# Optimization experiments

Measured on AMD Instinct MI355X. Metric: run time of the kernel, lower is better.

The kernel has to match this reference:

```python
import jax, jax.numpy as jnp
import numpy as np
from jax import lax

# Problem dims (match init_kwargs / input_specs)
B, C, H, W = 4, 256, 64, 64
G, KH, KW, PAD = 8, 3, 3, 1
KK = KH * KW
CG = C // G  # channels per group


def setup_inputs() -> dict:
    key = jax.random.key(0)
    k0, k1, k2, k3, k4 = jax.random.split(key, 5)
    x = jax.random.normal(k0, (B, C, H, W), jnp.float32)
    # offset predictor conv: Conv2d(C, 2*KK*G, 3, padding=1); small init keeps offsets moderate
    offset_w = jax.random.normal(k1, (2 * KK * G, C, 3, 3), jnp.float32) * 0.01
    offset_b = jax.random.normal(k2, (2 * KK * G,), jnp.float32) * 0.01
    # deformable grouped conv weight: [C_out=C, C_in//G, KH, KW]
    fan_in = CG * KK
    deform_w = jax.random.normal(k3, (C, CG, KH, KW), jnp.float32) / np.sqrt(fan_in).astype(np.float32)
    deform_b = jax.random.normal(k4, (C,), jnp.float32) * 0.01
    return {"x": x, "offset_w": offset_w, "offset_b": offset_b,
            "deform_w": deform_w, "deform_b": deform_b}


def _deform_group_conv(x, offset_w, offset_b, deform_w, deform_b):
    # 1) predict offsets with a plain 3x3 conv
    offset = lax.conv_general_dilated(
        x, offset_w, window_strides=(1, 1), padding=((PAD, PAD), (PAD, PAD)),
        dimension_numbers=("NCHW", "OIHW", "NCHW")) + offset_b[None, :, None, None]

    # torchvision layout: [B, G, KK, (dy,dx), H, W]
    off = offset.reshape(B, G, KK, 2, H, W)
    off_y, off_x = off[:, :, :, 0], off[:, :, :, 1]  # [B,G,KK,H,W]

    dt = x.dtype
    hh = jnp.arange(H, dtype=dt)[None, None, None, :, None]
    ww = jnp.arange(W, dtype=dt)[None, None, None, None, :]
    ki = (jnp.arange(KK) // KW).astype(dt)[None, None, :, None, None]
    kj = (jnp.arange(KK) % KW).astype(dt)[None, None, :, None, None]
    # sampling coords for each (kernel tap, output location): [B,G,KK,H,W]
    py = hh - PAD + ki + off_y
    px = ww - PAD + kj + off_x

    y0f, x0f = jnp.floor(py), jnp.floor(px)
    wy1, wx1 = py - y0f, px - x0f
    wy0, wx0 = 1.0 - wy1, 1.0 - wx1
    iy0, ix0 = y0f.astype(jnp.int32), x0f.astype(jnp.int32)

    x_g = x.reshape(B, G, CG, H * W)
    # gather over flattened spatial dim, vmapped over (B, G)
    gather = jax.vmap(jax.vmap(lambda xf, idx: jnp.take(xf, idx, axis=1)))

    def corner(iy, ix, wgt):
        valid = (iy >= 0) & (iy < H) & (ix >= 0) & (ix < W)  # zero padding outside
        idx = (jnp.clip(iy, 0, H - 1) * W + jnp.clip(ix, 0, W - 1)).reshape(B, G, -1)
        w = (wgt * valid.astype(wgt.dtype)).reshape(B, G, 1, -1)
        return gather(x_g, idx) * w  # [B,G,CG,KK*H*W]

    sampled = (corner(iy0,     ix0,     wy0 * wx0)
             + corner(iy0,     ix0 + 1, wy0 * wx1)
             + corner(iy0 + 1, ix0,     wy1 * wx0)
             + corner(iy0 + 1, ix0 + 1, wy1 * wx1))
    sampled = sampled.reshape(B, G, CG, KK, H, W)

    # grouped conv as an einsum over (in-channels-per-group, kernel taps)
    w_g = deform_w.reshape(G, C // G, CG, KK)  # [G, out/g, in/g, KK]
    out = jnp.einsum("gock,bgckhw->bgohw", w_g, sampled).reshape(B, C, H, W)
    return out + deform_b[None, :, None, None]


def reference(x, offset_w, offset_b, deform_w, deform_b):
    return _deform_group_conv(x, offset_w, offset_b, deform_w, deform_b)
```

## Files before the change

kernel.cpp:

```cpp
#include <hip/hip_runtime.h>
#include <hip/hip_bf16.h>
#include <cstddef>
#include <cstdint>

#define CH_HW 4096

typedef __bf16  bf16x8  __attribute__((ext_vector_type(8)));
typedef float   f32x4   __attribute__((ext_vector_type(4)));
typedef unsigned int u32x4 __attribute__((ext_vector_type(4)));

#define WF_ELEMS 331776
#define WF_BYTES (WF_ELEMS * 2)
#define OFFW_BYTES (4u * 144u * CH_HW * 2u)
#define DWB_ELEMS (8 * 9 * 2 * 512)
#define DWB_BYTES (DWB_ELEMS * 2)
#define XT_BYTES ((size_t)4 * 8 * CH_HW * 32 * 2)

__device__ __forceinline__ u32x4 pack_bf16x8(const float av[8]) {
    u32x4 ad;
#pragma unroll
    for (int jj = 0; jj < 4; ++jj) {
        const unsigned int lo = __builtin_bit_cast(unsigned short, __float2bfloat16(av[2 * jj]));
        const unsigned int hi = __builtin_bit_cast(unsigned short, __float2bfloat16(av[2 * jj + 1]));
        ad[jj] = lo | (hi << 16);
    }
    return ad;
}
__device__ __forceinline__ float bf16lo(unsigned int u) {
    return __builtin_bit_cast(float, u << 16);
}
__device__ __forceinline__ float bf16hi(unsigned int u) {
    return __builtin_bit_cast(float, u & 0xFFFF0000u);
}

__global__ __launch_bounds__(256) void prep(const float* __restrict__ ow,
                                            const float* __restrict__ dw,
                                            const float* __restrict__ x,
                                            __hip_bfloat16* __restrict__ wf,
                                            __hip_bfloat16* __restrict__ dwb,
                                            __hip_bfloat16* __restrict__ xt)
{
    const int job = blockIdx.y;
    if (job == 0) {
        const int t = blockIdx.x * 256 + threadIdx.x;
        if (t >= WF_ELEMS) return;
        const int j    = t & 7;
        const int lane = (t >> 3) & 63;
        const int tmp  = t >> 9;
        const int nt   = tmp % 9;
        const int ks   = tmp / 9;
        const int tap  = ks >> 3, icb = ks & 7;
        const int oc   = nt * 16 + (lane & 15);
        const int ic   = icb * 32 + (lane >> 4) * 8 + j;
        wf[t] = __float2bfloat16(ow[(size_t)oc * 2304 + ic * 9 + tap]);
    } else if (job == 1) {
        const int t = blockIdx.x * 256 + threadIdx.x;
        if (t >= DWB_ELEMS) return;
        const int j    = t & 7;
        const int lane = (t >> 3) & 63;
        const int nt   = (t >> 9) & 1;
        const int gk   = t >> 10;
        const int k    = gk % 9;
        const int g    = gk / 9;
        const int oc   = g * 32 + nt * 16 + (lane & 15);
        const int c    = (lane >> 4) * 8 + j;
        dwb[t] = __float2bfloat16(dw[(size_t)oc * 288 + c * 9 + k]);
    } else {
        const int bid = blockIdx.x;
        if (bid >= 512) return;
        const int chunk = bid & 15;
        const int g = (bid >> 4) & 7, b = bid >> 7;
        const int pix = (chunk << 8) + threadIdx.x;
        const float* xs = x + ((size_t)b * 256 + g * 32) * CH_HW + pix;
        __hip_bfloat16* xp = xt + ((size_t)b * 8 + g) * 4 * CH_HW * 8;
#pragma unroll
        for (int q = 0; q < 4; ++q) {
            float av[8];
#pragma unroll
            for (int j = 0; j < 8; ++j) av[j] = xs[(size_t)(q * 8 + j) * CH_HW];
            *(u32x4*)(xp + ((size_t)q * CH_HW + pix) * 8) = pack_bf16x8(av);
        }
    }
}

template<int NT>
__device__ __forceinline__ void offs_body7(
    const __hip_bfloat16* __restrict__ xb,
    const __hip_bfloat16* __restrict__ wfl,
    const float* __restrict__ ob,
    __hip_bfloat16* __restrict__ offw_b,
    float* __restrict__ red,
    int hrow, int lane, int ntBase, int kh)
{
    const int arow = lane & 15, cgrp = lane >> 4;
    const int ks0 = kh * 18;

    auto loadA1 = [&](int ks, int mt) -> u32x4 {
        const int tap = ks >> 3, icb = ks & 7;
        const int dy = tap / 3 - 1, dx = tap % 3 - 1;
        const int sh = hrow + dy, sw = mt * 16 + arow + dx;
        const bool valid = (sh >= 0) & (sh < 64) & (sw >= 0) & (sw < 64);
        const int spix = (min(max(sh, 0), 63) << 6) + min(max(sw, 0), 63);
        u32x4 a = *(const u32x4*)(xb + ((size_t)(icb * 4 + cgrp) * CH_HW + spix) * 8);
        if (!valid) a = (u32x4){0, 0, 0, 0};
        return a;
    };

    f32x4 acc[4][NT];
#pragma unroll
    for (int mt = 0; mt < 4; ++mt)
#pragma unroll
        for (int nt = 0; nt < NT; ++nt) acc[mt][nt] = (f32x4){0.f, 0.f, 0.f, 0.f};

    u32x4 a0[4], a1[4], b0[NT], b1[NT];
#pragma unroll
    for (int mt = 0; mt < 4; ++mt) {
        a0[mt] = loadA1(ks0 + 0, mt);
        a1[mt] = loadA1(ks0 + 1, mt);
    }
#pragma unroll
    for (int nt = 0; nt < NT; ++nt) {
        b0[nt] = *(const u32x4*)(wfl + (size_t)((ks0 + 0) * 9 + nt) * 512);
        b1[nt] = *(const u32x4*)(wfl + (size_t)((ks0 + 1) * 9 + nt) * 512);
    }

#pragma unroll 1
    for (int i = 0; i < 16; i += 2) {
        const int ks = ks0 + i;
#pragma unroll
        for (int mt = 0; mt < 4; ++mt) {
            const bf16x8 af = __builtin_bit_cast(bf16x8, a0[mt]);
#pragma unroll
            for (int nt = 0; nt < NT; ++nt)
                acc[mt][nt] = __builtin_amdgcn_mfma_f32_16x16x32_bf16(
                    af, __builtin_bit_cast(bf16x8, b0[nt]), acc[mt][nt], 0, 0, 0);
        }
#pragma unroll
        for (int mt = 0; mt < 4; ++mt) a0[mt] = loadA1(ks + 2, mt);
#pragma unroll
        for (int nt = 0; nt < NT; ++nt)
            b0[nt] = *(const u32x4*)(wfl + (size_t)((ks + 2) * 9 + nt) * 512);
#pragma unroll
        for (int mt = 0; mt < 4; ++mt) {
            const bf16x8 af = __builtin_bit_cast(bf16x8, a1[mt]);
#pragma unroll
            for (int nt = 0; nt < NT; ++nt)
                acc[mt][nt] = __builtin_amdgcn_mfma_f32_16x16x32_bf16(
                    af, __builtin_bit_cast(bf16x8, b1[nt]), acc[mt][nt], 0, 0, 0);
        }
#pragma unroll
        for (int mt = 0; mt < 4; ++mt) a1[mt] = loadA1(ks + 3, mt);
#pragma unroll
        for (int nt = 0; nt < NT; ++nt)
            b1[nt] = *(const u32x4*)(wfl + (size_t)((ks + 3) * 9 + nt) * 512);
    }
#pragma unroll
    for (int mt = 0; mt < 4; ++mt) {
        const bf16x8 af = __builtin_bit_cast(bf16x8, a0[mt]);
#pragma unroll
        for (int nt = 0; nt < NT; ++nt)
            acc[mt][nt] = __builtin_amdgcn_mfma_f32_16x16x32_bf16(
                af, __builtin_bit_cast(bf16x8, b0[nt]), acc[mt][nt], 0, 0, 0);
    }
#pragma unroll
    for (int mt = 0; mt < 4; ++mt) {
        const bf16x8 af = __builtin_bit_cast(bf16x8, a1[mt]);
#pragma unroll
        for (int nt = 0; nt < NT; ++nt)
            acc[mt][nt] = __builtin_amdgcn_mfma_f32_16x16x32_bf16(
                af, __builtin_bit_cast(bf16x8, b1[nt]), acc[mt][nt], 0, 0, 0);
    }

    const int RSTRIDE = 1024 * NT;
    if (kh > 0) {
        float* r = red + (kh - 1) * RSTRIDE;
#pragma unroll
        for (int mt = 0; mt < 4; ++mt)
#pragma unroll
            for (int nt = 0; nt < NT; ++nt)
                *(f32x4*)&r[((mt * NT + nt) * 64 + lane) * 4] = acc[mt][nt];
    }
    __syncthreads();
    if (kh == 0) {
#pragma unroll
        for (int mt = 0; mt < 4; ++mt) {
            const int pxb = hrow * 64 + mt * 16 + (cgrp << 2);
#pragma unroll
            for (int nt = 0; nt < NT; ++nt) {
                const int ri = ((mt * NT + nt) * 64 + lane) * 4;
                const f32x4 p1 = *(const f32x4*)&red[ri];
                const f32x4 p2 = *(const f32x4*)&red[RSTRIDE + ri];
                const f32x4 p3 = *(const f32x4*)&red[2 * RSTRIDE + ri];
                const int oc = (ntBase + nt) * 16 + arow;
                const float bias = ob[oc];
                float av[4];
#pragma unroll
                for (int r4 = 0; r4 < 4; ++r4)
                    av[r4] = acc[mt][nt][r4] + p1[r4] + p2[r4] + p3[r4] + bias;
                unsigned int q0 = (unsigned int)__builtin_bit_cast(unsigned short, __float2bfloat16(av[0])) |
                                  ((unsigned int)__builtin_bit_cast(unsigned short, __float2bfloat16(av[1])) << 16);
                unsigned int q1 = (unsigned int)__builtin_bit_cast(unsigned short, __float2bfloat16(av[2])) |
                                  ((unsigned int)__builtin_bit_cast(unsigned short, __float2bfloat16(av[3])) << 16);
                unsigned int* op = (unsigned int*)(offw_b + (size_t)oc * CH_HW + pxb);
                op[0] = q0; op[1] = q1;
            }
        }
    }
}

__global__ __launch_bounds__(256, 2) void offs_mfma7(
    const __hip_bfloat16* __restrict__ xt,
    const __hip_bfloat16* __restrict__ wf,
    const float* __restrict__ ob,
    __hip_bfloat16* __restrict__ offw)
{
    __shared__ float red[15360];
    const int bid  = blockIdx.x;
    const int xcd  = bid & 7;
    const int b    = xcd >> 1;
    const int half = xcd & 1;
    const int q    = bid >> 3;
    const int hrow = q;
    const int nh   = half;
    const int tid  = threadIdx.x;
    const int lane = tid & 63, kh = tid >> 6;
    const int ntBase = nh * 5;

    const __hip_bfloat16* xb  = xt + (size_t)b * 8 * CH_HW * 32;
    const __hip_bfloat16* wfl = wf + (size_t)(ntBase * 64 + lane) * 8;
    __hip_bfloat16* offw_b = offw + (size_t)b * 144 * CH_HW;

    if (nh == 0) offs_body7<5>(xb, wfl, ob, offw_b, red, hrow, lane, ntBase, kh);
    else         offs_body7<4>(xb, wfl, ob, offw_b, red, hrow, lane, ntBase, kh);
}

struct Samp { int iA, iB, iC, iD; float wA, wB, wC, wD; };

__device__ __forceinline__ Samp make_samp(float py, float px) {
    const float y0f = floorf(py), x0f = floorf(px);
    const int iy0 = (int)y0f, ix0 = (int)x0f;
    const int iy1 = iy0 + 1,  ix1 = ix0 + 1;
    const float fy1 = py - y0f, fx1 = px - x0f;
    const float fy0 = 1.f - fy1, fx0 = 1.f - fx1;
    const bool vy0 = (iy0 >= 0) & (iy0 < 64);
    const bool vy1 = (iy1 >= 0) & (iy1 < 64);
    const bool vx0 = (ix0 >= 0) & (ix0 < 64);
    const bool vx1 = (ix1 >= 0) & (ix1 < 64);
    const int cy0 = min(max(iy0, 0), 63), cy1 = min(max(iy1, 0), 63);
    const int cx0 = min(max(ix0, 0), 63), cx1 = min(max(ix1, 0), 63);
    Samp s;
    s.iA = (cy0 << 6) + cx0; s.iB = (cy0 << 6) + cx1;
    s.iC = (cy1 << 6) + cx0; s.iD = (cy1 << 6) + cx1;
    s.wA = (vy0 & vx0) ? fy0 * fx0 : 0.f;
    s.wB = (vy0 & vx1) ? fy0 * fx1 : 0.f;
    s.wC = (vy1 & vx0) ? fy1 * fx0 : 0.f;
    s.wD = (vy1 & vx1) ? fy1 * fx1 : 0.f;
    return s;
}

__global__ __launch_bounds__(256, 4) void deform6(
    const __hip_bfloat16* __restrict__ xt,
    const __hip_bfloat16* __restrict__ offw,
    const __hip_bfloat16* __restrict__ dwb,
    const float* __restrict__ db,
    float* __restrict__ out)
{
    const int bid  = blockIdx.x;
    const int pair = bid & 31;
    const int pt   = bid >> 5;
    const int b    = pair >> 3;
    const int g    = pair & 7;
    const int tid = threadIdx.x;
    const int lane = tid & 63, wave = tid >> 6;
    const int arow = lane & 15, cgrp = lane >> 4;
    const int px = (pt << 6) + (wave << 4) + arow;
    const int h = px >> 6, w = px & 63;

    const __hip_bfloat16* xg   = xt + (((size_t)b * 8 + g) * 4 + cgrp) * CH_HW * 8;
    const __hip_bfloat16* offp = offw + ((size_t)b * 144 + g * 18) * CH_HW + px;
    const __hip_bfloat16* wgb  = dwb + (size_t)g * 9 * 2 * 512 + lane * 8;

    f32x4 acc0 = (f32x4){0.f, 0.f, 0.f, 0.f};
    f32x4 acc1 = (f32x4){0.f, 0.f, 0.f, 0.f};

#pragma unroll
    for (int k = 0; k < 9; ++k) {
        const float oy = __bfloat162float(offp[(size_t)(2 * k) * CH_HW]);
        const float ox = __bfloat162float(offp[(size_t)(2 * k + 1) * CH_HW]);
        const Samp s = make_samp((float)(h - 1 + k / 3) + oy,
                                 (float)(w - 1 + k % 3) + ox);
        const u32x4 cA = *(const u32x4*)(xg + (size_t)s.iA * 8);
        const u32x4 cB = *(const u32x4*)(xg + (size_t)s.iB * 8);
        const u32x4 cC = *(const u32x4*)(xg + (size_t)s.iC * 8);
        const u32x4 cD = *(const u32x4*)(xg + (size_t)s.iD * 8);
        const u32x4 bu0 = *(const u32x4*)(wgb + (size_t)(k * 2 + 0) * 512);
        const u32x4 bu1 = *(const u32x4*)(wgb + (size_t)(k * 2 + 1) * 512);

        float v[8];
#pragma unroll
        for (int qq = 0; qq < 4; ++qq) {
            v[2 * qq] = s.wA * bf16lo(cA[qq]) + s.wB * bf16lo(cB[qq]) +
                        s.wC * bf16lo(cC[qq]) + s.wD * bf16lo(cD[qq]);
            v[2 * qq + 1] = s.wA * bf16hi(cA[qq]) + s.wB * bf16hi(cB[qq]) +
                            s.wC * bf16hi(cC[qq]) + s.wD * bf16hi(cD[qq]);
        }
        const bf16x8 afr = __builtin_bit_cast(bf16x8, pack_bf16x8(v));
        acc0 = __builtin_amdgcn_mfma_f32_16x16x32_bf16(
            afr, __builtin_bit_cast(bf16x8, bu0), acc0, 0, 0, 0);
        acc1 = __builtin_amdgcn_mfma_f32_16x16x32_bf16(
            afr, __builtin_bit_cast(bf16x8, bu1), acc1, 0, 0, 0);
    }

    const int pix4 = (pt << 6) + (wave << 4) + (cgrp << 2);
#pragma unroll
    for (int nt = 0; nt < 2; ++nt) {
        const f32x4 a = nt ? acc1 : acc0;
        const int oc = g * 32 + nt * 16 + arow;
        const float bias = db[oc];
        float4 o4;
        o4.x = a[0] + bias; o4.y = a[1] + bias;
        o4.z = a[2] + bias; o4.w = a[3] + bias;
        *(float4*)&out[((size_t)b * 256 + oc) * CH_HW + pix4] = o4;
    }
}

__device__ __forceinline__ void stageA_load(const float* __restrict__ xb,
                                            int hrow, int m, int kc, int ks,
                                            float av[8])
{
    const int tap = ks >> 3, icb = ks & 7;
    const int dy = tap / 3 - 1, dx = tap % 3 - 1;
    const int sh = hrow + dy, sw = m + dx;
    const float msk = (sh >= 0 && sh < 64 && sw >= 0 && sw < 64) ? 1.f : 0.f;
    const int shc = min(max(sh, 0), 63), swc = min(max(sw, 0), 63);
    const float* p = xb + (size_t)(icb * 32 + kc * 8) * CH_HW + (shc << 6) + swc;
#pragma unroll
    for (int j = 0; j < 8; ++j) av[j] = p[(size_t)j * CH_HW] * msk;
}

__global__ __launch_bounds__(256) void offs_mfma(const float* __restrict__ x,
                                                 const __hip_bfloat16* __restrict__ wf,
                                                 const float* __restrict__ ob,
                                                 __hip_bfloat16* __restrict__ offw)
{
    __shared__ __align__(16) unsigned short aL[2][64][40];
    __shared__ __align__(16) unsigned short bL[2][2560];

    const int bid  = blockIdx.x;
    const int nh   = bid & 1;
    const int hrow = (bid >> 1) & 63;
    const int b    = bid >> 7;
    const int ntBase = nh * 5;
    const int NTLOC  = 5 - nh;
    const int tid  = threadIdx.x;
    const int lane = tid & 63, wave = tid >> 6;
    const int m    = lane;
    const int kc   = wave;

    const float* xb = x + (size_t)b * 256 * CH_HW;

    f32x4 acc[5];
#pragma unroll
    for (int q = 0; q < 5; ++q) acc[q] = (f32x4){0.f, 0.f, 0.f, 0.f};

    {
        float av[8]; u32x4 bv[2];
        stageA_load(xb, hrow, m, kc, 0, av);
#pragma unroll
        for (int q = 0; q < 2; ++q) {
            const int ntl = wave + q * 4;
            if (ntl < NTLOC)
                bv[q] = *(const u32x4*)(wf + ((size_t)(ntBase + ntl) * 64 + lane) * 8);
        }
        *(u32x4*)&aL[0][m][kc * 8] = pack_bf16x8(av);
#pragma unroll
        for (int q = 0; q < 2; ++q) {
            const int ntl = wave + q * 4;
            if (ntl < NTLOC) *(u32x4*)&bL[0][ntl * 512 + lane * 8] = bv[q];
        }
    }
    __syncthreads();

    for (int ks = 0; ks < 72; ++ks) {
        const int buf = ks & 1, nbuf = buf ^ 1;
        const bool hasNext = (ks + 1) < 72;

        float av[8]; u32x4 bv[2];
        if (hasNext) {
            stageA_load(xb, hrow, m, kc, ks + 1, av);
#pragma unroll
            for (int q = 0; q < 2; ++q) {
                const int ntl = wave + q * 4;
                if (ntl < NTLOC)
                    bv[q] = *(const u32x4*)(wf + ((size_t)((ks + 1) * 9 + ntBase + ntl) * 64 + lane) * 8);
            }
        }

        const u32x4 au = *(const u32x4*)&aL[buf][wave * 16 + (lane & 15)][(lane >> 4) * 8];
        const bf16x8 afr = __builtin_bit_cast(bf16x8, au);
#pragma unroll
        for (int ntl = 0; ntl < 5; ++ntl) {
            if (ntl < NTLOC) {
                const u32x4 bu = *(const u32x4*)&bL[buf][ntl * 512 + lane * 8];
                acc[ntl] = __builtin_amdgcn_mfma_f32_16x16x32_bf16(
                    afr, __builtin_bit_cast(bf16x8, bu), acc[ntl], 0, 0, 0);
            }
        }

        if (hasNext) {
            *(u32x4*)&aL[nbuf][m][kc * 8] = pack_bf16x8(av);
#pragma unroll
            for (int q = 0; q < 2; ++q) {
                const int ntl = wave + q * 4;
                if (ntl < NTLOC) *(u32x4*)&bL[nbuf][ntl * 512 + lane * 8] = bv[q];
            }
        }
        __syncthreads();
    }

    const int oc_l = lane & 15;
    const int mrow = wave * 16 + ((lane >> 4) << 2);
#pragma unroll
    for (int ntl = 0; ntl < 5; ++ntl) {
        if (ntl < NTLOC) {
            const int oc = (ntBase + ntl) * 16 + oc_l;
            const float bias = ob[oc];
            __hip_bfloat16* op = offw + ((size_t)b * 144 + oc) * CH_HW + hrow * 64 + mrow;
#pragma unroll
            for (int r = 0; r < 4; ++r)
                op[r] = __float2bfloat16(acc[ntl][r] + bias);
        }
    }
}

__global__ __launch_bounds__(256) void deform3(const float* __restrict__ x,
                                               const __hip_bfloat16* __restrict__ offw,
                                               const __hip_bfloat16* __restrict__ dwb,
                                               const float* __restrict__ db,
                                               float* __restrict__ out)
{
    const int pt = blockIdx.x;
    const int g  = blockIdx.y;
    const int b  = blockIdx.z;
    const int tid  = threadIdx.x;
    const int lane = tid & 63, wave = tid >> 6;
    const int pixbase = (pt << 7) + (wave << 5);
    const int arow = lane & 15;
    const int cgrp = lane >> 4;

    const float* xg = x + ((size_t)b * 256 + g * 32 + cgrp * 8) * CH_HW;
    const __hip_bfloat16* offp = offw + ((size_t)b * 144 + g * 18) * CH_HW;
    const __hip_bfloat16* wgb = dwb + (size_t)g * 9 * 2 * 512;

    f32x4 acc[2][2];
#pragma unroll
    for (int mt = 0; mt < 2; ++mt)
#pragma unroll
        for (int nt = 0; nt < 2; ++nt) acc[mt][nt] = (f32x4){0.f, 0.f, 0.f, 0.f};

#pragma unroll 1
    for (int k = 0; k < 9; ++k) {
        const u32x4 bu0 = *(const u32x4*)(wgb + (size_t)(k * 2 + 0) * 512 + lane * 8);
        const u32x4 bu1 = *(const u32x4*)(wgb + (size_t)(k * 2 + 1) * 512 + lane * 8);
        const bf16x8 bf0 = __builtin_bit_cast(bf16x8, bu0);
        const bf16x8 bf1 = __builtin_bit_cast(bf16x8, bu1);
        const int ki = k / 3, kj = k % 3;

#pragma unroll
        for (int mt = 0; mt < 2; ++mt) {
            const int pix = pixbase + mt * 16 + arow;
            const int h = pix >> 6, w = pix & 63;
            const float oy = __bfloat162float(offp[(2 * k) * CH_HW + pix]);
            const float ox = __bfloat162float(offp[(2 * k + 1) * CH_HW + pix]);
            const Samp s = make_samp((float)(h - 1 + ki) + oy,
                                     (float)(w - 1 + kj) + ox);
            float v[8];
#pragma unroll
            for (int j = 0; j < 8; ++j) {
                const float* xc = xg + (size_t)j * CH_HW;
                v[j] = s.wA * xc[s.iA] + s.wB * xc[s.iB] +
                       s.wC * xc[s.iC] + s.wD * xc[s.iD];
            }
            const bf16x8 afr = __builtin_bit_cast(bf16x8, pack_bf16x8(v));
            acc[mt][0] = __builtin_amdgcn_mfma_f32_16x16x32_bf16(afr, bf0, acc[mt][0], 0, 0, 0);
            acc[mt][1] = __builtin_amdgcn_mfma_f32_16x16x32_bf16(afr, bf1, acc[mt][1], 0, 0, 0);
        }
    }

    const int ocl = lane & 15;
#pragma unroll
    for (int mt = 0; mt < 2; ++mt)
#pragma unroll
        for (int nt = 0; nt < 2; ++nt) {
            const int oc = g * 32 + nt * 16 + ocl;
            const float bias = db[oc];
            const int pix = pixbase + mt * 16 + ((lane >> 4) << 2);
            float4 o4;
            o4.x = acc[mt][nt][0] + bias;
            o4.y = acc[mt][nt][1] + bias;
            o4.z = acc[mt][nt][2] + bias;
            o4.w = acc[mt][nt][3] + bias;
            *(float4*)&out[((size_t)b * 256 + oc) * CH_HW + pix] = o4;
        }
}

extern "C" void kernel_launch(void* const* d_in, const int* in_sizes, int n_in,
                              void* d_out, int out_size, void* d_ws, size_t ws_size,
                              hipStream_t stream) {
    const float* x  = (const float*)d_in[0];
    const float* ow = (const float*)d_in[1];
    const float* ob = (const float*)d_in[2];
    const float* dw = (const float*)d_in[3];
    const float* db = (const float*)d_in[4];
    float* out = (float*)d_out;

    __hip_bfloat16* wf   = (__hip_bfloat16*)d_ws;
    __hip_bfloat16* offw = (__hip_bfloat16*)((char*)d_ws + WF_BYTES);
    __hip_bfloat16* dwb  = (__hip_bfloat16*)((char*)d_ws + WF_BYTES + OFFW_BYTES);
    __hip_bfloat16* xt   = (__hip_bfloat16*)((char*)d_ws + WF_BYTES + OFFW_BYTES + DWB_BYTES);

    const size_t needed = (size_t)WF_BYTES + OFFW_BYTES + DWB_BYTES + XT_BYTES;
    const int nblk = (WF_ELEMS + 255) / 256;

    if (ws_size >= needed) {
        prep<<<dim3(nblk, 3, 1), 256, 0, stream>>>(ow, dw, x, wf, dwb, xt);
        offs_mfma7<<<512, 256, 0, stream>>>(xt, wf, ob, offw);
        deform6<<<2048, 256, 0, stream>>>(xt, offw, dwb, db, out);
    } else {
        prep<<<dim3(nblk, 2, 1), 256, 0, stream>>>(ow, dw, x, wf, dwb, xt);
        offs_mfma<<<512, 256, 0, stream>>>(x, wf, ob, offw);
        deform3<<<dim3(32, 8, 4), 256, 0, stream>>>(x, offw, dwb, db, out);
    }
}
```

Before: 53.98 us.

## Store offsets pixel-interleaved and process two pixel tiles per deform wave

The offset conv now writes its bf16 output as [b][g][pixel][18] instead of channel-planar, so the deform kernel can load all 18 offsets for a pixel with a few wide loads rather than 18 strided scalar loads. The deform kernel (deform7) has each wave handle two 16-pixel tiles, reusing the per-tap weight fragments across both MFMA pairs, and the grid is halved. In exchange, the offset kernel's epilogue becomes scattered 2-byte stores with stride 18, and the vector loads at 36-byte pixel strides are not 16-byte aligned.

```diff
diff --git a/kernel.cpp b/kernel.cpp
--- a/kernel.cpp
+++ b/kernel.cpp
@@ -88,7 +88,7 @@
     const __hip_bfloat16* __restrict__ xb,
     const __hip_bfloat16* __restrict__ wfl,
     const float* __restrict__ ob,
-    __hip_bfloat16* __restrict__ offw_b,
+    __hip_bfloat16* __restrict__ offw2_b,
     float* __restrict__ red,
     int hrow, int lane, int ntBase, int kh)
 {
@@ -192,17 +192,15 @@
                 const f32x4 p2 = *(const f32x4*)&red[RSTRIDE + ri];
                 const f32x4 p3 = *(const f32x4*)&red[2 * RSTRIDE + ri];
                 const int oc = (ntBase + nt) * 16 + arow;
+                const int g  = oc / 18;
+                const int ocl = oc - g * 18;
                 const float bias = ob[oc];
-                float av[4];
-#pragma unroll
-                for (int r4 = 0; r4 < 4; ++r4)
-                    av[r4] = acc[mt][nt][r4] + p1[r4] + p2[r4] + p3[r4] + bias;
-                unsigned int q0 = (unsigned int)__builtin_bit_cast(unsigned short, __float2bfloat16(av[0])) |
-                                  ((unsigned int)__builtin_bit_cast(unsigned short, __float2bfloat16(av[1])) << 16);
-                unsigned int q1 = (unsigned int)__builtin_bit_cast(unsigned short, __float2bfloat16(av[2])) |
-                                  ((unsigned int)__builtin_bit_cast(unsigned short, __float2bfloat16(av[3])) << 16);
-                unsigned int* op = (unsigned int*)(offw_b + (size_t)oc * CH_HW + pxb);
-                op[0] = q0; op[1] = q1;
+                __hip_bfloat16* op = offw2_b + ((size_t)g * CH_HW + pxb) * 18 + ocl;
+#pragma unroll
+                for (int r4 = 0; r4 < 4; ++r4) {
+                    const float v = acc[mt][nt][r4] + p1[r4] + p2[r4] + p3[r4] + bias;
+                    op[(size_t)r4 * 18] = __float2bfloat16(v);
+                }
             }
         }
     }
@@ -212,15 +210,14 @@
     const __hip_bfloat16* __restrict__ xt,
     const __hip_bfloat16* __restrict__ wf,
     const float* __restrict__ ob,
-    __hip_bfloat16* __restrict__ offw)
+    __hip_bfloat16* __restrict__ offw2)
 {
     __shared__ float red[15360];
     const int bid  = blockIdx.x;
     const int xcd  = bid & 7;
     const int b    = xcd >> 1;
     const int half = xcd & 1;
-    const int q    = bid >> 3;
-    const int hrow = q;
+    const int hrow = bid >> 3;
     const int nh   = half;
     const int tid  = threadIdx.x;
     const int lane = tid & 63, kh = tid >> 6;
@@ -228,10 +225,10 @@
 
     const __hip_bfloat16* xb  = xt + (size_t)b * 8 * CH_HW * 32;
     const __hip_bfloat16* wfl = wf + (size_t)(ntBase * 64 + lane) * 8;
-    __hip_bfloat16* offw_b = offw + (size_t)b * 144 * CH_HW;
-
-    if (nh == 0) offs_body7<5>(xb, wfl, ob, offw_b, red, hrow, lane, ntBase, kh);
-    else         offs_body7<4>(xb, wfl, ob, offw_b, red, hrow, lane, ntBase, kh);
+    __hip_bfloat16* offw2_b = offw2 + (size_t)b * 8 * CH_HW * 18;
+
+    if (nh == 0) offs_body7<5>(xb, wfl, ob, offw2_b, red, hrow, lane, ntBase, kh);
+    else         offs_body7<4>(xb, wfl, ob, offw2_b, red, hrow, lane, ntBase, kh);
 }
 
 struct Samp { int iA, iB, iC, iD; float wA, wB, wC, wD; };
@@ -258,9 +255,31 @@
     return s;
 }
 
-__global__ __launch_bounds__(256, 4) void deform6(
+__device__ __forceinline__ f32x4 bilin8(const __hip_bfloat16* xg, const Samp& s,
+                                        const bf16x8 bfr0, const bf16x8 bfr1,
+                                        f32x4 acc0, f32x4 acc1, f32x4* acc1out)
+{
+    const u32x4 cA = *(const u32x4*)(xg + (size_t)s.iA * 8);
+    const u32x4 cB = *(const u32x4*)(xg + (size_t)s.iB * 8);
+    const u32x4 cC = *(const u32x4*)(xg + (size_t)s.iC * 8);
+    const u32x4 cD = *(const u32x4*)(xg + (size_t)s.iD * 8);
+    float v[8];
+#pragma unroll
+    for (int qq = 0; qq < 4; ++qq) {
+        v[2 * qq] = s.wA * bf16lo(cA[qq]) + s.wB * bf16lo(cB[qq]) +
+                    s.wC * bf16lo(cC[qq]) + s.wD * bf16lo(cD[qq]);
+        v[2 * qq + 1] = s.wA * bf16hi(cA[qq]) + s.wB * bf16hi(cB[qq]) +
+                        s.wC * bf16hi(cC[qq]) + s.wD * bf16hi(cD[qq]);
+    }
+    const bf16x8 afr = __builtin_bit_cast(bf16x8, pack_bf16x8(v));
+    acc0 = __builtin_amdgcn_mfma_f32_16x16x32_bf16(afr, bfr0, acc0, 0, 0, 0);
+    *acc1out = __builtin_amdgcn_mfma_f32_16x16x32_bf16(afr, bfr1, acc1, 0, 0, 0);
+    return acc0;
+}
+
+__global__ __launch_bounds__(256, 4) void deform7(
     const __hip_bfloat16* __restrict__ xt,
-    const __hip_bfloat16* __restrict__ offw,
+    const __hip_bfloat16* __restrict__ offw2,
     const __hip_bfloat16* __restrict__ dwb,
     const float* __restrict__ db,
     float* __restrict__ out)
@@ -273,54 +292,70 @@
     const int tid = threadIdx.x;
     const int lane = tid & 63, wave = tid >> 6;
     const int arow = lane & 15, cgrp = lane >> 4;
-    const int px = (pt << 6) + (wave << 4) + arow;
-    const int h = px >> 6, w = px & 63;
-
-    const __hip_bfloat16* xg   = xt + (((size_t)b * 8 + g) * 4 + cgrp) * CH_HW * 8;
-    const __hip_bfloat16* offp = offw + ((size_t)b * 144 + g * 18) * CH_HW + px;
-    const __hip_bfloat16* wgb  = dwb + (size_t)g * 9 * 2 * 512 + lane * 8;
-
-    f32x4 acc0 = (f32x4){0.f, 0.f, 0.f, 0.f};
-    f32x4 acc1 = (f32x4){0.f, 0.f, 0.f, 0.f};
+    const int wbase = (pt << 7) + (wave << 5);
+    const int px0 = wbase + arow;
+    const int px1 = wbase + 16 + arow;
+    const int h0 = px0 >> 6, w0 = px0 & 63;
+    const int h1 = px1 >> 6, w1 = px1 & 63;
+
+    const __hip_bfloat16* xg  = xt + (((size_t)b * 8 + g) * 4 + cgrp) * CH_HW * 8;
+    const __hip_bfloat16* wgb = dwb + (size_t)g * 9 * 2 * 512 + lane * 8;
+    const __hip_bfloat16* obase = offw2 + ((size_t)b * 8 + g) * CH_HW * 18;
+
+    unsigned int po0[9], po1[9];
+    {
+        const unsigned int* p0 = (const unsigned int*)(obase + (size_t)px0 * 18);
+        const unsigned int* p1 = (const unsigned int*)(obase + (size_t)px1 * 18);
+        const u32x4 a0 = *(const u32x4*)p0;
+        const u32x4 a1 = *(const u32x4*)(p0 + 4);
+        const unsigned int a2 = p0[8];
+        const u32x4 c0 = *(const u32x4*)p1;
+        const u32x4 c1 = *(const u32x4*)(p1 + 4);
+        const unsigned int c2 = p1[8];
+#pragma unroll
+        for (int k = 0; k < 4; ++k) { po0[k] = a0[k]; po0[k + 4] = a1[k]; }
+        po0[8] = a2;
+#pragma unroll
+        for (int k = 0; k < 4; ++k) { po1[k] = c0[k]; po1[k + 4] = c1[k]; }
+        po1[8] = c2;
+    }
+
+    f32x4 acc[2][2];
+#pragma unroll
+    for (int mt = 0; mt < 2; ++mt)
+#pragma unroll
+        for (int nt = 0; nt < 2; ++nt) acc[mt][nt] = (f32x4){0.f, 0.f, 0.f, 0.f};
 
 #pragma unroll
     for (int k = 0; k < 9; ++k) {
-        const float oy = __bfloat162float(offp[(size_t)(2 * k) * CH_HW]);
-        const float ox = __bfloat162float(offp[(size_t)(2 * k + 1) * CH_HW]);
-        const Samp s = make_samp((float)(h - 1 + k / 3) + oy,
-                                 (float)(w - 1 + k % 3) + ox);
-        const u32x4 cA = *(const u32x4*)(xg + (size_t)s.iA * 8);
-        const u32x4 cB = *(const u32x4*)(xg + (size_t)s.iB * 8);
-        const u32x4 cC = *(const u32x4*)(xg + (size_t)s.iC * 8);
-        const u32x4 cD = *(const u32x4*)(xg + (size_t)s.iD * 8);
-        const u32x4 bu0 = *(const u32x4*)(wgb + (size_t)(k * 2 + 0) * 512);
-        const u32x4 bu1 = *(const u32x4*)(wgb + (size_t)(k * 2 + 1) * 512);
-
-        float v[8];
-#pragma unroll
-        for (int qq = 0; qq < 4; ++qq) {
-            v[2 * qq] = s.wA * bf16lo(cA[qq]) + s.wB * bf16lo(cB[qq]) +
-                        s.wC * bf16lo(cC[qq]) + s.wD * bf16lo(cD[qq]);
-            v[2 * qq + 1] = s.wA * bf16hi(cA[qq]) + s.wB * bf16hi(cB[qq]) +
-                            s.wC * bf16hi(cC[qq]) + s.wD * bf16hi(cD[qq]);
-        }
-        const bf16x8 afr = __builtin_bit_cast(bf16x8, pack_bf16x8(v));
-        acc0 = __builtin_amdgcn_mfma_f32_16x16x32_bf16(
-            afr, __builtin_bit_cast(bf16x8, bu0), acc0, 0, 0, 0);
-        acc1 = __builtin_amdgcn_mfma_f32_16x16x32_bf16(
-            afr, __builtin_bit_cast(bf16x8, bu1), acc1, 0, 0, 0);
-    }
-
-    const int pix4 = (pt << 6) + (wave << 4) + (cgrp << 2);
-#pragma unroll
-    for (int nt = 0; nt < 2; ++nt) {
-        const f32x4 a = nt ? acc1 : acc0;
-        const int oc = g * 32 + nt * 16 + arow;
-        const float bias = db[oc];
-        float4 o4;
-        o4.x = a[0] + bias; o4.y = a[1] + bias;
-        o4.z = a[2] + bias; o4.w = a[3] + bias;
-        *(float4*)&out[((size_t)b * 256 + oc) * CH_HW + pix4] = o4;
+        const bf16x8 bfr0 = __builtin_bit_cast(bf16x8,
+            *(const u32x4*)(wgb + (size_t)(k * 2 + 0) * 512));
+        const bf16x8 bfr1 = __builtin_bit_cast(bf16x8,
+            *(const u32x4*)(wgb + (size_t)(k * 2 + 1) * 512));
+        const int ki = k / 3, kj = k % 3;
+
+        const Samp s0 = make_samp((float)(h0 - 1 + ki) + bf16lo(po0[k]),
+                                  (float)(w0 - 1 + kj) + bf16hi(po0[k]));
+        acc[0][0] = bilin8(xg, s0, bfr0, bfr1, acc[0][0], acc[0][1], &acc[0][1]);
+
+        const Samp s1 = make_samp((float)(h1 - 1 + ki) + bf16lo(po1[k]),
+                                  (float)(w1 - 1 + kj) + bf16hi(po1[k]));
+        acc[1][0] = bilin8(xg, s1, bfr0, bfr1, acc[1][0], acc[1][1], &acc[1][1]);
+    }
+
+#pragma unroll
+    for (int mt = 0; mt < 2; ++mt) {
+        const int pix4 = wbase + mt * 16 + (cgrp << 2);
+#pragma unroll
+        for (int nt = 0; nt < 2; ++nt) {
+            const f32x4 a = acc[mt][nt];
+            const int oc = g * 32 + nt * 16 + arow;
+            const float bias = db[oc];
+            float4 o4;
+            o4.x = a[0] + bias; o4.y = a[1] + bias;
+            o4.z = a[2] + bias; o4.w = a[3] + bias;
+            *(float4*)&out[((size_t)b * 256 + oc) * CH_HW + pix4] = o4;
+        }
     }
 }
 
@@ -525,7 +560,7 @@
     if (ws_size >= needed) {
         prep<<<dim3(nblk, 3, 1), 256, 0, stream>>>(ow, dw, x, wf, dwb, xt);
         offs_mfma7<<<512, 256, 0, stream>>>(xt, wf, ob, offw);
-        deform6<<<2048, 256, 0, stream>>>(xt, offw, dwb, db, out);
+        deform7<<<1024, 256, 0, stream>>>(xt, offw, dwb, db, out);
     } else {
         prep<<<dim3(nblk, 2, 1), 256, 0, stream>>>(ow, dw, x, wf, dwb, xt);
         offs_mfma<<<512, 256, 0, stream>>>(x, wf, ob, offw);
```

New measurement: 52.51 us. 2.7% less time.
